# Optimization experiments

Hardware: AMD Instinct MI355X
Metric: run time of the kernel (lower is better)

Reference implementation:

```python
import jax, jax.numpy as jnp
import numpy as np

B, D, H, W, K = 16, 48, 256, 512, 2


def setup_inputs() -> dict:
    key = jax.random.key(0)
    cost = jax.random.normal(key, (B, D, H, W), dtype=jnp.float32)
    return {"cost": cost, "k": K}


def reference(cost, k):
    # cost: [B, D, H, W]; top-k over the disparity channel (dim 1).
    # Move D to the last axis for lax.top_k (equivalent to torch sort-desc + slice + gather).
    c = jnp.transpose(cost, (0, 2, 3, 1))            # [B, H, W, D]
    vals, idx = jax.lax.top_k(c, k)                  # [B, H, W, k] values & indices (desc)
    w = jax.nn.softmax(vals, axis=-1)                # softmax over the k selected costs
    disp = jnp.sum(w * idx.astype(cost.dtype), -1)   # expected disparity [B, H, W]
    return disp[:, None, :, :]                       # [B, 1, H, W]
```

## Files before the change

### kernel.cpp

```cpp
#include <hip/hip_runtime.h>
#include <math.h>

constexpr int B = 16, D = 48, H = 256, W = 512;
constexpr int HW = H * W;
constexpr int PIX = B * HW;
constexpr int VEC = 4;
constexpr int NTHREADS = PIX / VEC;

__global__ __launch_bounds__(256) void topk2_disp_kernel(
    const float* __restrict__ cost, float* __restrict__ out) {
    const int tid = blockIdx.x * blockDim.x + threadIdx.x;
    const int p   = tid << 2;
    const int b   = tid >> 15;
    const int rem = p & (HW - 1);

    const float* base = cost + (size_t)b * D * HW + rem;

    float v1[VEC], v2[VEC];
    int   i1[VEC], i2[VEC];
#pragma unroll
    for (int j = 0; j < VEC; ++j) {
        v1[j] = -INFINITY; v2[j] = -INFINITY; i1[j] = 0; i2[j] = 0;
    }

#pragma unroll
    for (int d = 0; d < D; ++d) {
        float4 v = *reinterpret_cast<const float4*>(base + (size_t)d * HW);
        float vv[VEC] = {v.x, v.y, v.z, v.w};
#pragma unroll
        for (int j = 0; j < VEC; ++j) {
            const float x = vv[j];
            if (x > v1[j]) {
                v2[j] = v1[j]; i2[j] = i1[j];
                v1[j] = x;     i1[j] = d;
            } else if (x > v2[j]) {
                v2[j] = x;     i2[j] = d;
            }
        }
    }

    float4 o;
    float res[VEC];
#pragma unroll
    for (int j = 0; j < VEC; ++j) {
        const float e   = expf(v2[j] - v1[j]);
        const float inv = 1.0f / (1.0f + e);
        res[j] = ((float)i1[j] + e * (float)i2[j]) * inv;
    }
    o.x = res[0]; o.y = res[1]; o.z = res[2]; o.w = res[3];
    *reinterpret_cast<float4*>(out + p) = o;
}

extern "C" void kernel_launch(void* const* d_in, const int* in_sizes, int n_in,
                              void* d_out, int out_size, void* d_ws, size_t ws_size,
                              hipStream_t stream) {
    const float* cost = (const float*)d_in[0];
    float* out = (float*)d_out;

    constexpr int BLOCK = 256;
    constexpr int GRID  = NTHREADS / BLOCK;
    topk2_disp_kernel<<<GRID, BLOCK, 0, stream>>>(cost, out);
}
```

Before: 85.20 us.

## Pipeline disparity loads through LDS with async global_load_lds ring buffer

Replaces direct per-thread float4 global loads with a 4-slot LDS ring buffer filled by asynchronous global_load_lds, gated by explicit vmcnt waits. Each thread now handles 8 pixels across two float4 chunks, and outputs use nontemporal stores. The goal is to keep more memory requests in flight and hide latency on a bandwidth-bound streaming scan. In exchange it uses 32KB of LDS per block, which may reduce occupancy, and it relies on hand-written waitcnt ordering.

```diff
diff --git a/kernel.cpp b/kernel.cpp
--- a/kernel.cpp
+++ b/kernel.cpp
@@ -4,51 +4,94 @@
 constexpr int B = 16, D = 48, H = 256, W = 512;
 constexpr int HW = H * W;
 constexpr int PIX = B * HW;
-constexpr int VEC = 4;
-constexpr int NTHREADS = PIX / VEC;
+constexpr int BLOCK = 256;
+constexpr int PXB = 2048;
+constexpr int SLOTS = 4;
+constexpr int GRID = PIX / PXB;
 
-__global__ __launch_bounds__(256) void topk2_disp_kernel(
+typedef float f32x4 __attribute__((ext_vector_type(4)));
+
+template <int N>
+__device__ __forceinline__ void waitvm() {
+    asm volatile("s_waitcnt vmcnt(%0)" ::"i"(N) : "memory");
+}
+__device__ __forceinline__ void waitlgkm0() {
+    asm volatile("s_waitcnt lgkmcnt(0)" ::: "memory");
+}
+
+#define GLD_LDS16(gp, lp)                                          \
+    __builtin_amdgcn_global_load_lds(                              \
+        (const __attribute__((address_space(1))) void*)(gp),      \
+        (__attribute__((address_space(3))) void*)(lp), 16, 0, 0)
+
+__global__ __launch_bounds__(BLOCK) void topk2_disp_kernel(
     const float* __restrict__ cost, float* __restrict__ out) {
-    const int tid = blockIdx.x * blockDim.x + threadIdx.x;
-    const int p   = tid << 2;
-    const int b   = tid >> 15;
-    const int rem = p & (HW - 1);
+    __shared__ __align__(16) float lds[SLOTS * PXB];
 
-    const float* base = cost + (size_t)b * D * HW + rem;
+    const int t = threadIdx.x;
+    const int w = t >> 6;
+    const int l = t & 63;
+    const int pbase = blockIdx.x * PXB;
+    const int b = pbase >> 17;
+    const int rem = pbase & (HW - 1);
 
-    float v1[VEC], v2[VEC];
-    int   i1[VEC], i2[VEC];
+    const int lofs = w * 512 + l * 4;
+    const float* gsrc = cost + (size_t)b * D * HW + rem + lofs;
+    float* lwb = &lds[w * 512];
+
+    float v1[8], v2[8];
+    int i1[8], i2[8];
 #pragma unroll
-    for (int j = 0; j < VEC; ++j) {
+    for (int j = 0; j < 8; ++j) {
         v1[j] = -INFINITY; v2[j] = -INFINITY; i1[j] = 0; i2[j] = 0;
     }
 
 #pragma unroll
-    for (int d = 0; d < D; ++d) {
-        float4 v = *reinterpret_cast<const float4*>(base + (size_t)d * HW);
-        float vv[VEC] = {v.x, v.y, v.z, v.w};
+    for (int s = 0; s < SLOTS; ++s) {
+        const float* g = gsrc + (size_t)s * HW;
+        GLD_LDS16(g,       lwb + s * PXB);
+        GLD_LDS16(g + 256, lwb + s * PXB + 256);
+    }
+
+    auto consume = [&](int d, int slot) {
+        const f32x4 A  = *reinterpret_cast<const f32x4*>(&lds[slot * PXB + lofs]);
+        const f32x4 Bv = *reinterpret_cast<const f32x4*>(&lds[slot * PXB + lofs + 256]);
+        float x[8] = {A.x, A.y, A.z, A.w, Bv.x, Bv.y, Bv.z, Bv.w};
 #pragma unroll
-        for (int j = 0; j < VEC; ++j) {
-            const float x = vv[j];
-            if (x > v1[j]) {
+        for (int j = 0; j < 8; ++j) {
+            if (x[j] > v1[j]) {
                 v2[j] = v1[j]; i2[j] = i1[j];
-                v1[j] = x;     i1[j] = d;
-            } else if (x > v2[j]) {
-                v2[j] = x;     i2[j] = d;
+                v1[j] = x[j];  i1[j] = d;
+            } else if (x[j] > v2[j]) {
+                v2[j] = x[j];  i2[j] = d;
             }
         }
+    };
+
+    for (int d = 0; d < D - SLOTS; ++d) {
+        waitvm<2 * (SLOTS - 1)>();
+        consume(d, d & (SLOTS - 1));
+        waitlgkm0();
+        const float* g = gsrc + (size_t)(d + SLOTS) * HW;
+        GLD_LDS16(g,       lwb + (d & (SLOTS - 1)) * PXB);
+        GLD_LDS16(g + 256, lwb + (d & (SLOTS - 1)) * PXB + 256);
     }
+    waitvm<6>(); consume(44, 0);
+    waitvm<4>(); consume(45, 1);
+    waitvm<2>(); consume(46, 2);
+    waitvm<0>(); consume(47, 3);
 
-    float4 o;
-    float res[VEC];
+    float res[8];
 #pragma unroll
-    for (int j = 0; j < VEC; ++j) {
+    for (int j = 0; j < 8; ++j) {
         const float e   = expf(v2[j] - v1[j]);
         const float inv = 1.0f / (1.0f + e);
         res[j] = ((float)i1[j] + e * (float)i2[j]) * inv;
     }
-    o.x = res[0]; o.y = res[1]; o.z = res[2]; o.w = res[3];
-    *reinterpret_cast<float4*>(out + p) = o;
+    f32x4 o0 = {res[0], res[1], res[2], res[3]};
+    f32x4 o1 = {res[4], res[5], res[6], res[7]};
+    __builtin_nontemporal_store(o0, reinterpret_cast<f32x4*>(out + pbase + lofs));
+    __builtin_nontemporal_store(o1, reinterpret_cast<f32x4*>(out + pbase + lofs + 256));
 }
 
 extern "C" void kernel_launch(void* const* d_in, const int* in_sizes, int n_in,
@@ -56,8 +99,5 @@
                               hipStream_t stream) {
     const float* cost = (const float*)d_in[0];
     float* out = (float*)d_out;
-
-    constexpr int BLOCK = 256;
-    constexpr int GRID  = NTHREADS / BLOCK;
     topk2_disp_kernel<<<GRID, BLOCK, 0, stream>>>(cost, out);
 }
```

Result: slower. 105.9 us (+24.3%).
